# Optimization experiments

Measured on AMD Instinct MI355X. Metric: run time of the kernel, lower is better.

## Reference

```python
import jax, jax.numpy as jnp
import numpy as np

N = 32768       # batch of received vectors
N_RX = 8        # real-valued rx dimension (rows of G)
N_TX = 4        # n_tx_re
N_SYM = 4       # n_sym_re
K = N_SYM ** N_TX  # 256 joint symbol combos
SYMS = np.array([-3.0, -1.0, 1.0, 3.0]) / np.sqrt(5.0)  # 16-QAM real levels


def setup_inputs() -> dict:
    key = jax.random.key(0)
    k1, k2, k3, k4 = jax.random.split(key, 4)
    log_qi = jax.random.normal(k1, (N, N_TX, N_SYM), dtype=jnp.float32)
    G = jax.random.normal(k2, (N, N_RX, N_TX), dtype=jnp.float32)
    sqrt_2rho = jax.random.uniform(k3, (N,), dtype=jnp.float32, minval=0.5, maxval=2.0)
    n_var = jax.random.uniform(k4, (N,), dtype=jnp.float32, minval=0.05, maxval=0.5)
    # alpha is a NonNeg scalar weight (constant-initialized to 1.0). We use 0.8
    # (a plausible post-training value) so the (1-alpha)*log_qi path is exercised.
    alpha = jnp.float32(0.8)
    return {"log_qi": log_qi, "G": G, "sqrt_2rho": sqrt_2rho, "n_var": n_var, "alpha": alpha}


def _laplace_log_cdf(x):
    # Laplace(0,1): cdf = 0.5*exp(x) for x<0, 1 - 0.5*exp(-x) for x>=0
    return jnp.where(x < 0, x - jnp.log(2.0), jnp.log1p(-0.5 * jnp.exp(-jnp.abs(x))))


def reference(log_qi, G, sqrt_2rho, n_var, alpha):
    dt = log_qi.dtype
    syms = jnp.asarray(SYMS, dtype=dt)
    # All K = N_SYM**N_TX joint index combos (meshgrid 'ij' order = self.s_map order)
    grids = jnp.meshgrid(*([jnp.arange(N_SYM)] * N_TX), indexing='ij')
    idx = jnp.stack([g.reshape(-1) for g in grids], axis=-1)   # (K, N_TX) int
    s_all = syms[idx]                                          # (K, N_TX)

    # log p(y | s) for every joint combo: shared by all N_TX updates
    sG = sqrt_2rho[:, None, None] * G                          # (N, N_RX, N_TX)
    term = jnp.einsum('brt,kt->brk', sG, s_all)                # (N, N_RX, K)
    log_p = jnp.sum(_laplace_log_cdf(term), axis=1)            # (N, K)

    tx_ids = jnp.arange(N_TX)
    for xi in range(N_TX):  # unrolled Python loop, as in the original
        qi_un = jnp.exp(log_qi)
        qi = qi_un / jnp.sum(qi_un, axis=-1, keepdims=True)    # compute_qi
        # qi gathered at each combo: qi_sel[b,k,j] = qi[b, j, idx[k,j]]
        qi_sel = qi[:, tx_ids, idx]                            # (N, K, N_TX)
        # product over j != xi (row xi replaced by 1.0, as in tf.where insert)
        w = jnp.prod(jnp.where(tx_ids == xi, jnp.asarray(1.0, dt), qi_sel), axis=-1)  # (N, K)
        # group-sum combos by their xi-th symbol index
        onehot = (idx[:, xi][:, None] == jnp.arange(N_SYM)).astype(dt)  # (K, N_SYM)
        ex_log_qi = (w * log_p) @ onehot                       # (N, N_SYM)
        new_row = (1.0 - alpha) * log_qi[:, xi, :] + alpha * jax.lax.stop_gradient(ex_log_qi)
        log_qi = log_qi.at[:, xi, :].set(new_row)
        log_qi = log_qi - jax.lax.stop_gradient(jnp.max(log_qi, axis=-1, keepdims=True))
    return log_qi
```

## Files before the change

kernel.cpp:

```cpp
#include <hip/hip_runtime.h>

#define LOG2E 1.4426950408889634f
#define LN2F  0.6931471805599453f
#define RS5F  0.4472135954999579f

template<int XOR, int OR, int AND>
__device__ __forceinline__ float swz(float v) {
    return __int_as_float(__builtin_amdgcn_ds_swizzle(
        __float_as_int(v), (XOR << 10) | (OR << 5) | AND));
}
#define SWZX(v, m)    swz<(m), 0, 0x1F>(v)
#define BCAST32(v, s) swz<0, (s), 0>(v)
#define EXP2(x)  __builtin_amdgcn_exp2f(x)
#define LOG2_(x) __builtin_amdgcn_logf(x)
#define RCP_(x)  __builtin_amdgcn_rcpf(x)

__device__ __forceinline__ float sel4(float e0, float e1, float e2, float e3, int c) {
    float lo = (c & 1) ? e1 : e0;
    float hi = (c & 1) ? e3 : e2;
    return (c & 2) ? hi : lo;
}

__global__ __launch_bounds__(256, 8) void mfnet_layer_kernel(
    const float* __restrict__ log_qi,
    const float* __restrict__ G,
    const float* __restrict__ sqrt_2rho,
    const float* __restrict__ alpha_ptr,
    float* __restrict__ out,
    int N)
{
    const int tid  = threadIdx.x;
    const int wv   = tid >> 6;
    const int lane = tid & 63;
    const int grp  = lane >> 5;
    const int u    = lane & 31;
    const int ib   = blockIdx.x * 8 + wv * 2;

    __shared__ __align__(16) float sG[4][64];
    {
        size_t gidx = (size_t)ib * 32 + (size_t)lane;
        size_t gmax = (size_t)N * 32 - 1;
        if (gidx > gmax) gidx = gmax;
        sG[wv][lane] = G[gidx];
    }

    const int it0   = ib + grp;
    const bool valid = (it0 < N);
    const int item  = valid ? it0 : (N - 1);

    const float alpha = alpha_ptr[0];
    const float alm1  = 1.0f - alpha;

    const int bit0 = u & 1;
    const int c2   = (u >> 1) & 3;
    const int c1   = (u >> 3) & 3;

    const float rho = sqrt_2rho[item];
    const float rv  = rho * RS5F;
    const float s1  = rv * (float)(2 * c1 - 3);
    const float s2  = rv * (float)(2 * c2 - 3);
    const float w0  = rv * (float)(2 * bit0 - 3);

    float slq2[16];
    {
        const float4* lq = (const float4*)(log_qi + (size_t)item * 16);
#pragma unroll
        for (int i = 0; i < 4; ++i) {
            float4 v = lq[i];
            slq2[4*i+0] = v.x * LOG2E; slq2[4*i+1] = v.y * LOG2E;
            slq2[4*i+2] = v.z * LOG2E; slq2[4*i+3] = v.w * LOG2E;
        }
    }

    float q1A, q1C, q2A, q2C, q3v0, q3v1, q3v2, q3v3;
    {
        float e0 = EXP2(slq2[4]),  e1 = EXP2(slq2[5]);
        float e2 = EXP2(slq2[6]),  e3 = EXP2(slq2[7]);
        float inv = RCP_(e0 + e1 + e2 + e3);
        q1A = sel4(e0, e1, e2, e3, c1) * inv;
        q1C = sel4(e0, e1, e2, e3, c1 ^ 3) * inv;
    }
    {
        float e0 = EXP2(slq2[8]),  e1 = EXP2(slq2[9]);
        float e2 = EXP2(slq2[10]), e3 = EXP2(slq2[11]);
        float inv = RCP_(e0 + e1 + e2 + e3);
        q2A = sel4(e0, e1, e2, e3, c2) * inv;
        q2C = sel4(e0, e1, e2, e3, c2 ^ 3) * inv;
    }
    {
        float e0 = EXP2(slq2[12]), e1 = EXP2(slq2[13]);
        float e2 = EXP2(slq2[14]), e3 = EXP2(slq2[15]);
        float inv = RCP_(e0 + e1 + e2 + e3);
        q3v0 = e0*inv; q3v1 = e1*inv; q3v2 = e2*inv; q3v3 = e3*inv;
    }

    float lpA[4] = {0,0,0,0};
    float lpC[4] = {0,0,0,0};
    const float* gw = &sG[wv][grp * 32];
#pragma unroll
    for (int r = 0; r < 8; ++r) {
        float4 g = *(const float4*)(gw + r * 4);
        float tb = fmaf(g.x, w0, fmaf(g.y, s1, g.z * s2));
        float m3 = g.w * rv;
#pragma unroll
        for (int j = 0; j < 4; ++j) {
            float w3 = (float)(2 * j - 3);
            float x  = fmaf(m3, w3, tb);
            float tt = fabsf(x) * (-LOG2E);
            float e  = EXP2(tt);
            float lg = LOG2_(fmaf(e, -0.5f, 1.0f));
            float ng = tt - 1.0f;
            bool neg = (x < 0.0f);
            lpA[j] += neg ? ng : lg;
            lpC[j] += neg ? lg : ng;
        }
    }

    float UA = lpA[0]*q3v0 + lpA[1]*q3v1 + lpA[2]*q3v2 + lpA[3]*q3v3;
    float UC = lpC[0]*q3v3 + lpC[1]*q3v2 + lpC[2]*q3v1 + lpC[3]*q3v0;

    float q0A, q0C, IA, IC;
    {
        float SA = UA * (q1A * q2A);
        float SC = UC * (q1C * q2C);
        SA += SWZX(SA,2); SA += SWZX(SA,4); SA += SWZX(SA,8); SA += SWZX(SA,16);
        SC += SWZX(SC,2); SC += SWZX(SC,4); SC += SWZX(SC,8); SC += SWZX(SC,16);
        float SAo = SWZX(SA,1), SCo = SWZX(SC,1);
        float ex0 = bit0 ? SAo : SA;
        float ex1 = bit0 ? SA  : SAo;
        float ex2 = bit0 ? SC  : SCo;
        float ex3 = bit0 ? SCo : SC;
        slq2[0] = alm1*slq2[0] + alpha*ex0;
        slq2[1] = alm1*slq2[1] + alpha*ex1;
        slq2[2] = alm1*slq2[2] + alpha*ex2;
        slq2[3] = alm1*slq2[3] + alpha*ex3;
#pragma unroll
        for (int t = 0; t < 4; ++t) {
            float m = fmaxf(fmaxf(slq2[4*t], slq2[4*t+1]),
                            fmaxf(slq2[4*t+2], slq2[4*t+3]));
            slq2[4*t] -= m; slq2[4*t+1] -= m;
            slq2[4*t+2] -= m; slq2[4*t+3] -= m;
        }
        float e0 = EXP2(slq2[0]), e1 = EXP2(slq2[1]);
        float e2 = EXP2(slq2[2]), e3 = EXP2(slq2[3]);
        float inv = RCP_(e0 + e1 + e2 + e3);
        q0A = (bit0 ? e1 : e0) * inv;
        q0C = (bit0 ? e2 : e3) * inv;
        IA = q0A * UA;
        IC = q0C * UC;
    }

    {
        float SA = q2A * IA;
        float SC = q2C * IC;
        SA += SWZX(SA,1); SA += SWZX(SA,2); SA += SWZX(SA,4);
        SC += SWZX(SC,1); SC += SWZX(SC,2); SC += SWZX(SC,4);
        float T = SA + SWZX(SC, 24);
        float ex0 = BCAST32(T, 0),  ex1 = BCAST32(T, 8);
        float ex2 = BCAST32(T, 16), ex3 = BCAST32(T, 24);
        slq2[4] = alm1*slq2[4] + alpha*ex0;
        slq2[5] = alm1*slq2[5] + alpha*ex1;
        slq2[6] = alm1*slq2[6] + alpha*ex2;
        slq2[7] = alm1*slq2[7] + alpha*ex3;
        float m = fmaxf(fmaxf(slq2[4], slq2[5]), fmaxf(slq2[6], slq2[7]));
        slq2[4] -= m; slq2[5] -= m; slq2[6] -= m; slq2[7] -= m;
        float e0 = EXP2(slq2[4]), e1 = EXP2(slq2[5]);
        float e2 = EXP2(slq2[6]), e3 = EXP2(slq2[7]);
        float inv = RCP_(e0 + e1 + e2 + e3);
        q1A = sel4(e0, e1, e2, e3, c1) * inv;
        q1C = sel4(e0, e1, e2, e3, c1 ^ 3) * inv;
    }

    {
        float SA = q1A * IA;
        float SC = q1C * IC;
        SA += SWZX(SA,1); SA += SWZX(SA,8); SA += SWZX(SA,16);
        SC += SWZX(SC,1); SC += SWZX(SC,8); SC += SWZX(SC,16);
        float T = SA + SWZX(SC, 6);
        float ex0 = BCAST32(T, 0), ex1 = BCAST32(T, 2);
        float ex2 = BCAST32(T, 4), ex3 = BCAST32(T, 6);
        slq2[8]  = alm1*slq2[8]  + alpha*ex0;
        slq2[9]  = alm1*slq2[9]  + alpha*ex1;
        slq2[10] = alm1*slq2[10] + alpha*ex2;
        slq2[11] = alm1*slq2[11] + alpha*ex3;
        float m = fmaxf(fmaxf(slq2[8], slq2[9]), fmaxf(slq2[10], slq2[11]));
        slq2[8] -= m; slq2[9] -= m; slq2[10] -= m; slq2[11] -= m;
        float e0 = EXP2(slq2[8]),  e1 = EXP2(slq2[9]);
        float e2 = EXP2(slq2[10]), e3 = EXP2(slq2[11]);
        float inv = RCP_(e0 + e1 + e2 + e3);
        q2A = sel4(e0, e1, e2, e3, c2) * inv;
        q2C = sel4(e0, e1, e2, e3, c2 ^ 3) * inv;
    }

    {
        float WA = q0A * q1A * q2A;
        float WC = q0C * q1C * q2C;
        float R0 = lpA[0]*WA + lpC[3]*WC;
        float R1 = lpA[1]*WA + lpC[2]*WC;
        float R2 = lpA[2]*WA + lpC[1]*WC;
        float R3 = lpA[3]*WA + lpC[0]*WC;
        R0 += SWZX(R0,1); R0 += SWZX(R0,2); R0 += SWZX(R0,4); R0 += SWZX(R0,8); R0 += SWZX(R0,16);
        R1 += SWZX(R1,1); R1 += SWZX(R1,2); R1 += SWZX(R1,4); R1 += SWZX(R1,8); R1 += SWZX(R1,16);
        R2 += SWZX(R2,1); R2 += SWZX(R2,2); R2 += SWZX(R2,4); R2 += SWZX(R2,8); R2 += SWZX(R2,16);
        R3 += SWZX(R3,1); R3 += SWZX(R3,2); R3 += SWZX(R3,4); R3 += SWZX(R3,8); R3 += SWZX(R3,16);
        slq2[12] = alm1*slq2[12] + alpha*R0;
        slq2[13] = alm1*slq2[13] + alpha*R1;
        slq2[14] = alm1*slq2[14] + alpha*R2;
        slq2[15] = alm1*slq2[15] + alpha*R3;
        float m = fmaxf(fmaxf(slq2[12], slq2[13]), fmaxf(slq2[14], slq2[15]));
        slq2[12] -= m; slq2[13] -= m; slq2[14] -= m; slq2[15] -= m;
    }

    if (valid && u < 16) {
        const int c = u & 3;
        float r0 = sel4(slq2[0],  slq2[1],  slq2[2],  slq2[3],  c);
        float r1 = sel4(slq2[4],  slq2[5],  slq2[6],  slq2[7],  c);
        float r2 = sel4(slq2[8],  slq2[9],  slq2[10], slq2[11], c);
        float r3 = sel4(slq2[12], slq2[13], slq2[14], slq2[15], c);
        float vv = sel4(r0, r1, r2, r3, u >> 2);
        out[(size_t)item * 16 + u] = vv * LN2F;
    }
}

extern "C" void kernel_launch(void* const* d_in, const int* in_sizes, int n_in,
                              void* d_out, int out_size, void* d_ws, size_t ws_size,
                              hipStream_t stream) {
    const float* log_qi = (const float*)d_in[0];
    const float* G      = (const float*)d_in[1];
    const float* rho    = (const float*)d_in[2];
    const float* alpha  = (const float*)d_in[4];
    float* out = (float*)d_out;

    const int N = in_sizes[2];
    const int blocks = (N + 7) / 8;
    mfnet_layer_kernel<<<blocks, 256, 0, stream>>>(log_qi, G, rho, alpha, out, N);
}
```

Before: 84.63 us.

## Distribute log_qi state one element per lane with cross-lane softmax via bpermute

Each lane now holds a single log_qi element (lane&15 gives row and column) instead of a redundant 16-float copy in every lane. Softmax and max-normalisation are done with lane swizzles, and the needed q values are gathered with ds_bpermute. The LOG2E factor is folded into rv. The change targets redundant per-lane exp2, rcp and register work, at the cost of extra LDS-permute latency on the serial dependency chain.

```diff
diff --git a/kernel.cpp b/kernel.cpp
--- a/kernel.cpp
+++ b/kernel.cpp
@@ -9,11 +9,14 @@
     return __int_as_float(__builtin_amdgcn_ds_swizzle(
         __float_as_int(v), (XOR << 10) | (OR << 5) | AND));
 }
-#define SWZX(v, m)    swz<(m), 0, 0x1F>(v)
-#define BCAST32(v, s) swz<0, (s), 0>(v)
+#define SWZX(v, m) swz<(m), 0, 0x1F>(v)
 #define EXP2(x)  __builtin_amdgcn_exp2f(x)
 #define LOG2_(x) __builtin_amdgcn_logf(x)
 #define RCP_(x)  __builtin_amdgcn_rcpf(x)
+
+__device__ __forceinline__ float bperm(int byte_addr, float v) {
+    return __int_as_float(__builtin_amdgcn_ds_bpermute(byte_addr, __float_as_int(v)));
+}
 
 __device__ __forceinline__ float sel4(float e0, float e1, float e2, float e3, int c) {
     float lo = (c & 1) ? e1 : e0;
@@ -54,48 +57,46 @@
     const int bit0 = u & 1;
     const int c2   = (u >> 1) & 3;
     const int c1   = (u >> 3) & 3;
-
-    const float rho = sqrt_2rho[item];
-    const float rv  = rho * RS5F;
-    const float s1  = rv * (float)(2 * c1 - 3);
-    const float s2  = rv * (float)(2 * c2 - 3);
-    const float w0  = rv * (float)(2 * bit0 - 3);
-
-    float slq2[16];
-    {
-        const float4* lq = (const float4*)(log_qi + (size_t)item * 16);
-#pragma unroll
-        for (int i = 0; i < 4; ++i) {
-            float4 v = lq[i];
-            slq2[4*i+0] = v.x * LOG2E; slq2[4*i+1] = v.y * LOG2E;
-            slq2[4*i+2] = v.z * LOG2E; slq2[4*i+3] = v.w * LOG2E;
-        }
-    }
-
-    float q1A, q1C, q2A, q2C, q3v0, q3v1, q3v2, q3v3;
-    {
-        float e0 = EXP2(slq2[4]),  e1 = EXP2(slq2[5]);
-        float e2 = EXP2(slq2[6]),  e3 = EXP2(slq2[7]);
-        float inv = RCP_(e0 + e1 + e2 + e3);
-        q1A = sel4(e0, e1, e2, e3, c1) * inv;
-        q1C = sel4(e0, e1, e2, e3, c1 ^ 3) * inv;
-    }
-    {
-        float e0 = EXP2(slq2[8]),  e1 = EXP2(slq2[9]);
-        float e2 = EXP2(slq2[10]), e3 = EXP2(slq2[11]);
-        float inv = RCP_(e0 + e1 + e2 + e3);
-        q2A = sel4(e0, e1, e2, e3, c2) * inv;
-        q2C = sel4(e0, e1, e2, e3, c2 ^ 3) * inv;
-    }
-    {
-        float e0 = EXP2(slq2[12]), e1 = EXP2(slq2[13]);
-        float e2 = EXP2(slq2[14]), e3 = EXP2(slq2[15]);
-        float inv = RCP_(e0 + e1 + e2 + e3);
-        q3v0 = e0*inv; q3v1 = e1*inv; q3v2 = e2*inv; q3v3 = e3*inv;
-    }
-
-    float lpA[4] = {0,0,0,0};
-    float lpC[4] = {0,0,0,0};
+    const int ue   = u & 15;
+    const int row  = ue >> 2;
+    const int col  = ue & 3;
+
+    const float rv = sqrt_2rho[item] * (RS5F * LOG2E);
+    const float s1 = rv * (float)(2 * c1 - 3);
+    const float s2 = rv * (float)(2 * c2 - 3);
+    const float w0 = rv * (float)(2 * bit0 - 3);
+
+    float slqD = log_qi[(size_t)item * 16 + ue] * LOG2E;
+    {
+        float m1 = fmaxf(slqD, SWZX(slqD, 1));
+        float m  = fmaxf(m1, SWZX(m1, 2));
+        slqD -= m;
+    }
+
+    auto softmax_all = [&](float s) {
+        float e = EXP2(s);
+        float t = e + SWZX(e, 1);
+        float den = t + SWZX(t, 2);
+        return e * RCP_(den);
+    };
+    float qD = softmax_all(slqD);
+
+    const int gbase = lane & 32;
+    const int aQ1A = (gbase + 4 + c1) << 2;
+    const int aQ1C = (gbase + 4 + (c1 ^ 3)) << 2;
+    const int aQ2A = (gbase + 8 + c2) << 2;
+    const int aQ2C = (gbase + 8 + (c2 ^ 3)) << 2;
+    const int aR1  = (gbase + (col << 3)) << 2;
+    const int aR2  = (gbase + (col << 1)) << 2;
+
+    float q1A = bperm(aQ1A, qD), q1C = bperm(aQ1C, qD);
+    float q2A = bperm(aQ2A, qD), q2C = bperm(aQ2C, qD);
+    const int a3 = (gbase + 12) << 2;
+    float q3v0 = bperm(a3, qD),      q3v1 = bperm(a3 + 4, qD);
+    float q3v2 = bperm(a3 + 8, qD),  q3v3 = bperm(a3 + 12, qD);
+
+    float lpA[4] = {0, 0, 0, 0};
+    float lpC[4] = {0, 0, 0, 0};
     const float* gw = &sG[wv][grp * 32];
 #pragma unroll
     for (int r = 0; r < 8; ++r) {
@@ -104,13 +105,12 @@
         float m3 = g.w * rv;
 #pragma unroll
         for (int j = 0; j < 4; ++j) {
-            float w3 = (float)(2 * j - 3);
-            float x  = fmaf(m3, w3, tb);
-            float tt = fabsf(x) * (-LOG2E);
-            float e  = EXP2(tt);
+            float t  = fmaf(m3, (float)(2 * j - 3), tb);
+            float at = -fabsf(t);
+            float e  = EXP2(at);
             float lg = LOG2_(fmaf(e, -0.5f, 1.0f));
-            float ng = tt - 1.0f;
-            bool neg = (x < 0.0f);
+            float ng = at - 1.0f;
+            bool neg = (t < 0.0f);
             lpA[j] += neg ? ng : lg;
             lpC[j] += neg ? lg : ng;
         }
@@ -125,76 +125,57 @@
         float SC = UC * (q1C * q2C);
         SA += SWZX(SA,2); SA += SWZX(SA,4); SA += SWZX(SA,8); SA += SWZX(SA,16);
         SC += SWZX(SC,2); SC += SWZX(SC,4); SC += SWZX(SC,8); SC += SWZX(SC,16);
-        float SAo = SWZX(SA,1), SCo = SWZX(SC,1);
-        float ex0 = bit0 ? SAo : SA;
-        float ex1 = bit0 ? SA  : SAo;
-        float ex2 = bit0 ? SC  : SCo;
-        float ex3 = bit0 ? SCo : SC;
-        slq2[0] = alm1*slq2[0] + alpha*ex0;
-        slq2[1] = alm1*slq2[1] + alpha*ex1;
-        slq2[2] = alm1*slq2[2] + alpha*ex2;
-        slq2[3] = alm1*slq2[3] + alpha*ex3;
-#pragma unroll
-        for (int t = 0; t < 4; ++t) {
-            float m = fmaxf(fmaxf(slq2[4*t], slq2[4*t+1]),
-                            fmaxf(slq2[4*t+2], slq2[4*t+3]));
-            slq2[4*t] -= m; slq2[4*t+1] -= m;
-            slq2[4*t+2] -= m; slq2[4*t+3] -= m;
-        }
-        float e0 = EXP2(slq2[0]), e1 = EXP2(slq2[1]);
-        float e2 = EXP2(slq2[2]), e3 = EXP2(slq2[3]);
-        float inv = RCP_(e0 + e1 + e2 + e3);
-        q0A = (bit0 ? e1 : e0) * inv;
-        q0C = (bit0 ? e2 : e3) * inv;
+        float SAo = SWZX(SA, 1), SCo = SWZX(SC, 1);
+        float A0 = bit0 ? SAo : SA;
+        float A1 = bit0 ? SA  : SAo;
+        float C1 = bit0 ? SC  : SCo;
+        float C0 = bit0 ? SCo : SC;
+        float exD = sel4(A0, A1, C1, C0, col);
+        float bl = fmaf(alm1, slqD, alpha * exD);
+        slqD = (row == 0) ? bl : slqD;
+        float m1 = fmaxf(slqD, SWZX(slqD, 1));
+        float m  = fmaxf(m1, SWZX(m1, 2));
+        slqD -= m;
+        qD = softmax_all(slqD);
+        q0A = bperm((gbase + bit0) << 2, qD);
+        q0C = bperm((gbase + (bit0 ^ 3)) << 2, qD);
         IA = q0A * UA;
         IC = q0C * UC;
     }
 
     {
-        float SA = q2A * IA;
-        float SC = q2C * IC;
+        float SA = q2A * IA, SC = q2C * IC;
         SA += SWZX(SA,1); SA += SWZX(SA,2); SA += SWZX(SA,4);
         SC += SWZX(SC,1); SC += SWZX(SC,2); SC += SWZX(SC,4);
         float T = SA + SWZX(SC, 24);
-        float ex0 = BCAST32(T, 0),  ex1 = BCAST32(T, 8);
-        float ex2 = BCAST32(T, 16), ex3 = BCAST32(T, 24);
-        slq2[4] = alm1*slq2[4] + alpha*ex0;
-        slq2[5] = alm1*slq2[5] + alpha*ex1;
-        slq2[6] = alm1*slq2[6] + alpha*ex2;
-        slq2[7] = alm1*slq2[7] + alpha*ex3;
-        float m = fmaxf(fmaxf(slq2[4], slq2[5]), fmaxf(slq2[6], slq2[7]));
-        slq2[4] -= m; slq2[5] -= m; slq2[6] -= m; slq2[7] -= m;
-        float e0 = EXP2(slq2[4]), e1 = EXP2(slq2[5]);
-        float e2 = EXP2(slq2[6]), e3 = EXP2(slq2[7]);
-        float inv = RCP_(e0 + e1 + e2 + e3);
-        q1A = sel4(e0, e1, e2, e3, c1) * inv;
-        q1C = sel4(e0, e1, e2, e3, c1 ^ 3) * inv;
-    }
-
-    {
-        float SA = q1A * IA;
-        float SC = q1C * IC;
+        float exD = bperm(aR1, T);
+        float bl = fmaf(alm1, slqD, alpha * exD);
+        slqD = (row == 1) ? bl : slqD;
+        float m1 = fmaxf(slqD, SWZX(slqD, 1));
+        float m  = fmaxf(m1, SWZX(m1, 2));
+        slqD -= m;
+        qD = softmax_all(slqD);
+        q1A = bperm(aQ1A, qD); q1C = bperm(aQ1C, qD);
+    }
+
+    {
+        float SA = q1A * IA, SC = q1C * IC;
         SA += SWZX(SA,1); SA += SWZX(SA,8); SA += SWZX(SA,16);
         SC += SWZX(SC,1); SC += SWZX(SC,8); SC += SWZX(SC,16);
         float T = SA + SWZX(SC, 6);
-        float ex0 = BCAST32(T, 0), ex1 = BCAST32(T, 2);
-        float ex2 = BCAST32(T, 4), ex3 = BCAST32(T, 6);
-        slq2[8]  = alm1*slq2[8]  + alpha*ex0;
-        slq2[9]  = alm1*slq2[9]  + alpha*ex1;
-        slq2[10] = alm1*slq2[10] + alpha*ex2;
-        slq2[11] = alm1*slq2[11] + alpha*ex3;
-        float m = fmaxf(fmaxf(slq2[8], slq2[9]), fmaxf(slq2[10], slq2[11]));
-        slq2[8] -= m; slq2[9] -= m; slq2[10] -= m; slq2[11] -= m;
-        float e0 = EXP2(slq2[8]),  e1 = EXP2(slq2[9]);
-        float e2 = EXP2(slq2[10]), e3 = EXP2(slq2[11]);
-        float inv = RCP_(e0 + e1 + e2 + e3);
-        q2A = sel4(e0, e1, e2, e3, c2) * inv;
-        q2C = sel4(e0, e1, e2, e3, c2 ^ 3) * inv;
-    }
-
-    {
-        float WA = q0A * q1A * q2A;
-        float WC = q0C * q1C * q2C;
+        float exD = bperm(aR2, T);
+        float bl = fmaf(alm1, slqD, alpha * exD);
+        slqD = (row == 2) ? bl : slqD;
+        float m1 = fmaxf(slqD, SWZX(slqD, 1));
+        float m  = fmaxf(m1, SWZX(m1, 2));
+        slqD -= m;
+        qD = softmax_all(slqD);
+        q2A = bperm(aQ2A, qD); q2C = bperm(aQ2C, qD);
+    }
+
+    {
+        float WA = q0A * (q1A * q2A);
+        float WC = q0C * (q1C * q2C);
         float R0 = lpA[0]*WA + lpC[3]*WC;
         float R1 = lpA[1]*WA + lpC[2]*WC;
         float R2 = lpA[2]*WA + lpC[1]*WC;
@@ -203,22 +184,16 @@
         R1 += SWZX(R1,1); R1 += SWZX(R1,2); R1 += SWZX(R1,4); R1 += SWZX(R1,8); R1 += SWZX(R1,16);
         R2 += SWZX(R2,1); R2 += SWZX(R2,2); R2 += SWZX(R2,4); R2 += SWZX(R2,8); R2 += SWZX(R2,16);
         R3 += SWZX(R3,1); R3 += SWZX(R3,2); R3 += SWZX(R3,4); R3 += SWZX(R3,8); R3 += SWZX(R3,16);
-        slq2[12] = alm1*slq2[12] + alpha*R0;
-        slq2[13] = alm1*slq2[13] + alpha*R1;
-        slq2[14] = alm1*slq2[14] + alpha*R2;
-        slq2[15] = alm1*slq2[15] + alpha*R3;
-        float m = fmaxf(fmaxf(slq2[12], slq2[13]), fmaxf(slq2[14], slq2[15]));
-        slq2[12] -= m; slq2[13] -= m; slq2[14] -= m; slq2[15] -= m;
+        float exD = sel4(R0, R1, R2, R3, col);
+        float bl = fmaf(alm1, slqD, alpha * exD);
+        slqD = (row == 3) ? bl : slqD;
+        float m1 = fmaxf(slqD, SWZX(slqD, 1));
+        float m  = fmaxf(m1, SWZX(m1, 2));
+        slqD -= m;
     }
 
     if (valid && u < 16) {
-        const int c = u & 3;
-        float r0 = sel4(slq2[0],  slq2[1],  slq2[2],  slq2[3],  c);
-        float r1 = sel4(slq2[4],  slq2[5],  slq2[6],  slq2[7],  c);
-        float r2 = sel4(slq2[8],  slq2[9],  slq2[10], slq2[11], c);
-        float r3 = sel4(slq2[12], slq2[13], slq2[14], slq2[15], c);
-        float vv = sel4(r0, r1, r2, r3, u >> 2);
-        out[(size_t)item * 16 + u] = vv * LN2F;
+        out[(size_t)item * 16 + ue] = slqD * LN2F;
     }
 }
 
```

Result: faster. 79.38 us (-6.2%).
